# Kernel tuning notes

Measured on AMD Instinct MI355X. Metric: run time of the kernel, lower is better.

The kernel has to match this reference:

```python
import jax, jax.numpy as jnp
import numpy as np

K = 2
HD = 1024
IN = 784
NPARAMS = K + 2**K - 1  # 5
TRIL_R = np.array([0, 1, 1])  # tril_indices(2,2)
TRIL_C = np.array([0, 0, 1])


def setup_inputs() -> dict:
    key = jax.random.key(0)
    ks = jax.random.split(key, 8)
    B, T = 4096, 32
    s = 0.02
    return {
        "x": jax.random.normal(ks[0], (B, IN), jnp.float32),
        "hx": jnp.zeros((B, HD), jnp.float32),
        "eps": jax.random.normal(ks[1], (T, B, K), jnp.float32),
        "W_ih": jax.random.normal(ks[2], (HD, IN), jnp.float32) * s,
        "b_ih": jax.random.normal(ks[3], (HD,), jnp.float32) * s,
        "W_hh": jax.random.normal(ks[4], (HD, HD), jnp.float32) * s,
        "b_hh": jax.random.normal(ks[5], (HD,), jnp.float32) * s,
        "fe_W": jax.random.normal(ks[6], (NPARAMS, HD), jnp.float32) * s,
        "fe_b": jax.random.normal(ks[7], (NPARAMS,), jnp.float32) * s,
        "num_ticks": T,
    }


def _forward(x, hx, eps, W_ih, b_ih, W_hh, b_hh, fe_W, fe_b):
    B = x.shape[0]
    x_proj = x @ W_ih.T + b_ih  # invariant across ticks: [B, HD]
    diag = jnp.arange(K)

    def step(h, eps_t):
        h = jnp.tanh(x_proj + h @ W_hh.T + b_hh)  # RNNCell
        fe = h @ fe_W.T + fe_b                    # [B, NPARAMS]
        mus = fe[:, :K]
        sigmas = fe[:, K:]
        L = jnp.zeros((B, K, K), fe.dtype).at[:, TRIL_R, TRIL_C].set(sigmas)
        L = L.at[:, diag, diag].set(jax.nn.softplus(L[:, diag, diag]))
        z = mus + jnp.einsum('bij,bj->bi', L, eps_t)  # reparameterized sample
        return h, (z, L)

    _, (zs, Ls) = jax.lax.scan(step, hx, eps)  # zs: [T,B,K], Ls: [T,B,K,K]
    zs = jnp.transpose(zs, (1, 2, 0))          # [B, K, T]
    Ls = jnp.transpose(Ls, (1, 2, 3, 0))       # [B, K, K, T]
    # NOTE: original code stacks all_zs for both `zs` and `mus` (faithful to source).
    return zs, zs, Ls


def reference(x, hx, eps, W_ih, b_ih, W_hh, b_hh, fe_W, fe_b, num_ticks):
    eps = eps[:num_ticks]
    return _forward(x, hx, eps, W_ih, b_ih, W_hh, b_hh, fe_W, fe_b)
```

## Files before the change

kernel.cpp:

```cpp
#include <hip/hip_runtime.h>
#include <hip/hip_bf16.h>
#include <stdint.h>

#define B_ROWS 4096
#define HD 1024
#define IN_DIM 784
#define IN_PAD 832
#define T_TICKS 32

typedef float f32x4 __attribute__((ext_vector_type(4)));
typedef short short8 __attribute__((ext_vector_type(8)));
typedef __hip_bfloat16 bf16;

#define ABUF 8192

__device__ __forceinline__ float b2f(short s) {
  unsigned u = ((unsigned)(unsigned short)s) << 16;
  float f; __builtin_memcpy(&f, &u, 4); return f;
}

__device__ __forceinline__ float softplus_f(float x) {
  if (x > 20.f) return x;
  return log1pf(expf(x));
}

__device__ __forceinline__ float tanh_fast(float x) {
  x = fminf(fmaxf(x, -15.f), 15.f);
  float e = __expf(2.f * x);
  return (e - 1.f) / (e + 1.f);
}

__device__ __forceinline__ void gload_lds16(const void* g, void* l) {
  __builtin_amdgcn_global_load_lds(
      (const __attribute__((address_space(1))) uint32_t*)g,
      (__attribute__((address_space(3))) uint32_t*)l, 16, 0, 0);
}

__global__ __launch_bounds__(256) void conv_pad_kernel(
    const float* __restrict__ src, bf16* __restrict__ dst,
    int rows, int scols, int dcols) {
  int idx = blockIdx.x * 256 + threadIdx.x;
  int total = rows * dcols;
  if (idx >= total) return;
  int r = idx / dcols, c = idx - r * dcols;
  float v = (c < scols) ? src[(size_t)r * scols + c] : 0.f;
  dst[idx] = __float2bfloat16(v);
}

__global__ __launch_bounds__(256) void pack_w(
    const float* __restrict__ src, bf16* __restrict__ dst,
    int nkt, int scols) {
  int gid = blockIdx.x * 256 + threadIdx.x;
  int lane = gid & 63, f = gid >> 6;
  int total = 16 * nkt * 2 * 4;
  if (f >= total) return;
  int n = f & 3;
  int rest = f >> 2;
  int ks = rest & 1;
  int rest2 = rest >> 1;
  int kt = rest2 % nkt;
  int wnny = rest2 / nkt;
  int r = lane & 15, q = lane >> 4;
  int row = wnny * 64 + n * 16 + r;
  int k0 = kt * 64 + ks * 32 + q * 8;
  short8 v;
#pragma unroll
  for (int e = 0; e < 8; ++e) {
    int c = k0 + e;
    float x = (c < scols) ? src[(size_t)row * scols + c] : 0.f;
    bf16 b = __float2bfloat16(x);
    v[e] = *(short*)&b;
  }
  *(short8*)((char*)dst + (size_t)f * 1024 + lane * 16) = v;
}

__global__ __launch_bounds__(256) void pack_fe(
    const float* __restrict__ feW, bf16* __restrict__ dst) {
  int gid = blockIdx.x * 256 + threadIdx.x;
  int lane = gid & 63, f = gid >> 6;
  if (f >= 32) return;
  int ks = f & 1, kt = f >> 1;
  int r = lane & 15, q = lane >> 4;
  int k0 = kt * 64 + ks * 32 + q * 8;
  short8 v;
#pragma unroll
  for (int e = 0; e < 8; ++e) {
    float x = (r < 5) ? feW[(size_t)r * HD + k0 + e] : 0.f;
    bf16 b = __float2bfloat16(x);
    v[e] = *(short*)&b;
  }
  *(short8*)((char*)dst + (size_t)f * 1024 + lane * 16) = v;
}

template<int KDIM, int MODE>
__global__ __launch_bounds__(256) void gemm_core(
    const bf16* __restrict__ A,
    const bf16* __restrict__ Bpk,
    const bf16* __restrict__ feP,
    const float* __restrict__ bias1, const float* __restrict__ bias2,
    const bf16* __restrict__ xp, bf16* __restrict__ xp_out,
    bf16* __restrict__ outH, float* __restrict__ feRaw, int tprev)
{
  __shared__ char lds[2 * ABUF];
  const int tid = threadIdx.x;
  const int lane = tid & 63, w = tid >> 6;
  const int wm = w & 1, wn = w >> 1;
  const int l3 = lane >> 3, l7 = lane & 7;
  const int gcol = l7 ^ l3;
  const int r = lane & 15, q = lane >> 4;
  const int r7 = r & 7;
  const int lane16 = lane * 16;
  const int ldaB = KDIM * 2;
  const int NK = KDIM / 64;

  int bid = blockIdx.x;
  int v = (bid & 7) * 64 + (bid >> 3);
  const int mx = v >> 3, ny = v & 7;
  const int bm0 = mx * 64, bn0 = ny * 128;

  const bool feW0 = (MODE == 1) && (ny < 4) && (w == 0);

  f32x4 acc[2][4] = {};
  f32x4 acc_fe = {};

  const char* Asrc = (const char*)A + (size_t)(bm0 + l3) * ldaB + gcol * 16;
  const char* Bkt  = (const char*)Bpk + (size_t)(ny * 2 + wn) * NK * 8192;

  short8 Be[8], Bo[8], Bef[2], Bof[2];

#define STAGEA(buf, k)                                                         \
  {                                                                            \
    const char* Ak = Asrc + (size_t)(k) * 128;                                 \
    _Pragma("unroll") for (int j = 0; j < 2; ++j) {                            \
      int iA = w * 2 + j;                                                      \
      gload_lds16(Ak + (size_t)iA * 8 * ldaB, lds + (buf) * ABUF + iA * 1024); \
    }                                                                          \
  }

#define ISSUEB(BS, BSf, k)                                                     \
  {                                                                            \
    const char* bp = Bkt + (size_t)(k) * 8192;                                 \
    _Pragma("unroll") for (int i = 0; i < 8; ++i)                              \
      BS[i] = *(const short8*)(bp + i * 1024 + lane16);                        \
    if (feW0) {                                                                \
      const char* fp = (const char*)feP + (size_t)(k) * 2048;                  \
      BSf[0] = *(const short8*)(fp + lane16);                                  \
      BSf[1] = *(const short8*)(fp + 1024 + lane16);                           \
    }                                                                          \
  }

#define ITER(kp, BSc, BScf, BSn, BSnf)                                         \
  {                                                                            \
    const int _k = (kp);                                                       \
    if (_k + 1 < NK) {                                                         \
      STAGEA((_k + 1) & 1, _k + 1);                                            \
      ISSUEB(BSn, BSnf, _k + 1);                                               \
    }                                                                          \
    const char* lAb = lds + (_k & 1) * ABUF;                                   \
    short8 af[2][2], af_fe[2];                                                 \
    _Pragma("unroll") for (int ks = 0; ks < 2; ++ks) {                         \
      int sw = ((ks * 4 + q) ^ r7) << 4;                                       \
      _Pragma("unroll") for (int m = 0; m < 2; ++m)                            \
        af[ks][m] = *(const short8*)(lAb + (wm * 32 + m * 16 + r) * 128 + sw); \
    }                                                                          \
    if (feW0) {                                                                \
      _Pragma("unroll") for (int ks = 0; ks < 2; ++ks) {                       \
        int sw = ((ks * 4 + q) ^ r7) << 4;                                     \
        af_fe[ks] = *(const short8*)(lAb + (ny * 16 + r) * 128 + sw);          \
      }                                                                        \
    }                                                                          \
    _Pragma("unroll") for (int ks = 0; ks < 2; ++ks)                           \
      _Pragma("unroll") for (int m = 0; m < 2; ++m)                            \
        _Pragma("unroll") for (int n = 0; n < 4; ++n)                          \
          acc[m][n] = __builtin_amdgcn_mfma_f32_16x16x32_bf16(                 \
              af[ks][m], BSc[ks * 4 + n], acc[m][n], 0, 0, 0);                 \
    if (feW0) {                                                                \
      acc_fe = __builtin_amdgcn_mfma_f32_16x16x32_bf16(af_fe[0], BScf[0], acc_fe, 0, 0, 0); \
      acc_fe = __builtin_amdgcn_mfma_f32_16x16x32_bf16(af_fe[1], BScf[1], acc_fe, 0, 0, 0); \
    }                                                                          \
    __syncthreads();                                                           \
  }

  STAGEA(0, 0);
  ISSUEB(Be, Bef, 0);
  __syncthreads();

#pragma unroll
  for (int kt = 0; kt + 1 < NK; kt += 2) {
    ITER(kt,     Be, Bef, Bo, Bof);
    ITER(kt + 1, Bo, Bof, Be, Bef);
  }
  if (NK & 1) {
    ITER(NK - 1, Be, Bef, Bo, Bof);
  }
#undef ITER
#undef ISSUEB
#undef STAGEA

#pragma unroll
  for (int m = 0; m < 2; ++m) {
#pragma unroll
    for (int n = 0; n < 4; ++n) {
      int col = bn0 + wn * 64 + n * 16 + r;
#pragma unroll
      for (int i = 0; i < 4; ++i) {
        int row = bm0 + wm * 32 + m * 16 + q * 4 + i;
        float vv = acc[m][n][i];
        if (MODE == 0) {
          xp_out[(size_t)row * HD + col] = __float2bfloat16(vv + bias1[col] + bias2[col]);
        } else {
          float val = tanh_fast(vv + b2f(*(const short*)&xp[(size_t)row * HD + col]));
          outH[(size_t)row * HD + col] = __float2bfloat16(val);
        }
      }
    }
  }
  if (feW0 && tprev >= 0 && r < 5) {
#pragma unroll
    for (int i = 0; i < 4; ++i) {
      int rowg = bm0 + ny * 16 + q * 4 + i;
      feRaw[((size_t)rowg * T_TICKS + tprev) * 5 + r] = acc_fe[i];
    }
  }
}

__global__ __launch_bounds__(256) void fe_last(
    const bf16* __restrict__ h, const float* __restrict__ feW,
    float* __restrict__ feRaw)
{
  int wid = threadIdx.x >> 6, lane = threadIdx.x & 63;
  int b = blockIdx.x * 4 + wid;
  const bf16* hr = h + (size_t)b * HD + lane * 16;
  short8 hv0 = *(const short8*)hr;
  short8 hv1 = *(const short8*)(hr + 8);
  float hvf[16];
#pragma unroll
  for (int e = 0; e < 8; ++e) { hvf[e] = b2f(hv0[e]); hvf[8 + e] = b2f(hv1[e]); }

  float a0 = 0, a1 = 0, a2 = 0, a3 = 0, a4 = 0;
  int col0 = lane * 16;
#pragma unroll
  for (int e = 0; e < 16; ++e) {
    float hv = hvf[e];
    int col = col0 + e;
    a0 += hv * feW[0 * HD + col];
    a1 += hv * feW[1 * HD + col];
    a2 += hv * feW[2 * HD + col];
    a3 += hv * feW[3 * HD + col];
    a4 += hv * feW[4 * HD + col];
  }
#pragma unroll
  for (int off = 32; off >= 1; off >>= 1) {
    a0 += __shfl_xor(a0, off);
    a1 += __shfl_xor(a1, off);
    a2 += __shfl_xor(a2, off);
    a3 += __shfl_xor(a3, off);
    a4 += __shfl_xor(a4, off);
  }
  if (lane == 0) {
    float* fr = feRaw + ((size_t)b * T_TICKS + (T_TICKS - 1)) * 5;
    fr[0] = a0; fr[1] = a1; fr[2] = a2; fr[3] = a3; fr[4] = a4;
  }
}

__global__ __launch_bounds__(256) void finish_kernel(
    const float* __restrict__ feRaw, const float* __restrict__ feB,
    const float* __restrict__ eps, float* __restrict__ out)
{
  int gid = blockIdx.x * 256 + threadIdx.x;
  if (gid >= B_ROWS * T_TICKS) return;
  int b = gid >> 5, t = gid & 31;
  const float* fr = feRaw + ((size_t)b * T_TICKS + t) * 5;
  float mu0 = fr[0] + feB[0], mu1 = fr[1] + feB[1];
  float L00 = softplus_f(fr[2] + feB[2]);
  float L10 = fr[3] + feB[3];
  float L11 = softplus_f(fr[4] + feB[4]);
  const float* ep = eps + ((size_t)t * B_ROWS + b) * 2;
  float e0 = ep[0], e1 = ep[1];
  float z0 = mu0 + L00 * e0;
  float z1 = mu1 + L10 * e0 + L11 * e1;

  float* zs0 = out;
  float* zs1 = out + (size_t)B_ROWS * 2 * T_TICKS;
  float* Ls  = out + (size_t)2 * B_ROWS * 2 * T_TICKS;
  size_t zb = (size_t)b * 2 * T_TICKS + t;
  zs0[zb] = z0; zs0[zb + T_TICKS] = z1;
  zs1[zb] = z0; zs1[zb + T_TICKS] = z1;
  size_t lb = (size_t)b * 4 * T_TICKS + t;
  Ls[lb] = L00;
  Ls[lb + T_TICKS] = 0.f;
  Ls[lb + 2 * T_TICKS] = L10;
  Ls[lb + 3 * T_TICKS] = L11;
}

extern "C" void kernel_launch(void* const* d_in, const int* in_sizes, int n_in,
                              void* d_out, int out_size, void* d_ws, size_t ws_size,
                              hipStream_t stream) {
  const float* x    = (const float*)d_in[0];
  const float* hx   = (const float*)d_in[1];
  const float* eps  = (const float*)d_in[2];
  const float* W_ih = (const float*)d_in[3];
  const float* b_ih = (const float*)d_in[4];
  const float* W_hh = (const float*)d_in[5];
  const float* b_hh = (const float*)d_in[6];
  const float* fe_W = (const float*)d_in[7];
  const float* fe_b = (const float*)d_in[8];
  float* out = (float*)d_out;

  const int NKT_HH = HD / 64;
  const int NKT_IH = IN_PAD / 64;
  const int FR_HH = 16 * NKT_HH * 2 * 4;
  const int FR_IH = 16 * NKT_IH * 2 * 4;

  char* ws = (char*)d_ws;
  bf16* x_bf    = (bf16*)ws;  ws += (size_t)B_ROWS * IN_PAD * 2;
  bf16* hA      = (bf16*)ws;  ws += (size_t)B_ROWS * HD * 2;
  bf16* hB      = (bf16*)ws;  ws += (size_t)B_ROWS * HD * 2;
  bf16* xp_bf   = (bf16*)ws;  ws += (size_t)B_ROWS * HD * 2;
  bf16* pk_hh   = (bf16*)ws;  ws += (size_t)FR_HH * 1024;
  bf16* pk_ih   = (bf16*)ws;  ws += (size_t)FR_IH * 1024;
  bf16* feP     = (bf16*)ws;  ws += (size_t)32 * 1024;
  float* feRaw  = (float*)ws; ws += (size_t)B_ROWS * T_TICKS * 5 * 4;

  conv_pad_kernel<<<(B_ROWS * IN_PAD + 255) / 256, 256, 0, stream>>>(x, x_bf, B_ROWS, IN_DIM, IN_PAD);
  conv_pad_kernel<<<(B_ROWS * HD + 255) / 256, 256, 0, stream>>>(hx, hA, B_ROWS, HD, HD);
  pack_w<<<(FR_HH * 64 + 255) / 256, 256, 0, stream>>>(W_hh, pk_hh, NKT_HH, HD);
  pack_w<<<(FR_IH * 64 + 255) / 256, 256, 0, stream>>>(W_ih, pk_ih, NKT_IH, IN_DIM);
  pack_fe<<<(32 * 64 + 255) / 256, 256, 0, stream>>>(fe_W, feP);

  gemm_core<IN_PAD, 0><<<512, 256, 0, stream>>>(
      x_bf, pk_ih, nullptr, b_ih, b_hh,
      nullptr, xp_bf, nullptr, nullptr, -1);

  for (int t = 0; t < T_TICKS; ++t) {
    const bf16* hin = (t & 1) ? hB : hA;
    bf16* hout      = (t & 1) ? hA : hB;
    gemm_core<HD, 1><<<512, 256, 0, stream>>>(
        hin, pk_hh, feP, nullptr, nullptr,
        xp_bf, nullptr, hout, feRaw, t - 1);
  }
  fe_last<<<B_ROWS / 4, 256, 0, stream>>>(hA, fe_W, feRaw);
  finish_kernel<<<(B_ROWS * T_TICKS + 255) / 256, 256, 0, stream>>>(feRaw, fe_b, eps, out);
}
```

Baseline: 590.8 us.

## Use 128x128 tiles with intra-block split-K for the recurrent tick GEMM

Splits the per-tick recurrent GEMM into its own kernel. Each block now covers a 128x128 output tile with 512 threads instead of 64x128 with 256, and the grid shrinks from 512 to 256 blocks. The two halves of the waves each take half of every 64-wide K step, and their partial sums are reduced through LDS before the tanh epilogue. The aim is more reuse of A and B per block and less global traffic per output. The costs are a larger LDS footprint, an extra reduction pass, and fewer blocks in flight.

```diff
diff --git a/kernel.cpp b/kernel.cpp
--- a/kernel.cpp
+++ b/kernel.cpp
@@ -13,6 +13,8 @@
 typedef __hip_bfloat16 bf16;
 
 #define ABUF 8192
+#define TABUF 16384
+#define TLDS 66560
 
 __device__ __forceinline__ float b2f(short s) {
   unsigned u = ((unsigned)(unsigned short)s) << 16;
@@ -92,14 +94,12 @@
   *(short8*)((char*)dst + (size_t)f * 1024 + lane * 16) = v;
 }
 
-template<int KDIM, int MODE>
-__global__ __launch_bounds__(256) void gemm_core(
+template<int KDIM>
+__global__ __launch_bounds__(256) void gemm_xproj(
     const bf16* __restrict__ A,
     const bf16* __restrict__ Bpk,
-    const bf16* __restrict__ feP,
     const float* __restrict__ bias1, const float* __restrict__ bias2,
-    const bf16* __restrict__ xp, bf16* __restrict__ xp_out,
-    bf16* __restrict__ outH, float* __restrict__ feRaw, int tprev)
+    bf16* __restrict__ xp_out)
 {
   __shared__ char lds[2 * ABUF];
   const int tid = threadIdx.x;
@@ -118,108 +118,180 @@
   const int mx = v >> 3, ny = v & 7;
   const int bm0 = mx * 64, bn0 = ny * 128;
 
-  const bool feW0 = (MODE == 1) && (ny < 4) && (w == 0);
-
   f32x4 acc[2][4] = {};
-  f32x4 acc_fe = {};
-
   const char* Asrc = (const char*)A + (size_t)(bm0 + l3) * ldaB + gcol * 16;
   const char* Bkt  = (const char*)Bpk + (size_t)(ny * 2 + wn) * NK * 8192;
 
-  short8 Be[8], Bo[8], Bef[2], Bof[2];
-
-#define STAGEA(buf, k)                                                         \
-  {                                                                            \
-    const char* Ak = Asrc + (size_t)(k) * 128;                                 \
+  short8 Be[8], Bo[8];
+
+#define XSTAGE(buf, k)                                                         \
+  { const char* Ak = Asrc + (size_t)(k) * 128;                                 \
     _Pragma("unroll") for (int j = 0; j < 2; ++j) {                            \
       int iA = w * 2 + j;                                                      \
-      gload_lds16(Ak + (size_t)iA * 8 * ldaB, lds + (buf) * ABUF + iA * 1024); \
-    }                                                                          \
-  }
-
-#define ISSUEB(BS, BSf, k)                                                     \
-  {                                                                            \
-    const char* bp = Bkt + (size_t)(k) * 8192;                                 \
+      gload_lds16(Ak + (size_t)iA * 8 * ldaB, lds + (buf) * ABUF + iA * 1024); } }
+
+#define XISSUE(BS, k)                                                          \
+  { const char* bp = Bkt + (size_t)(k) * 8192;                                 \
     _Pragma("unroll") for (int i = 0; i < 8; ++i)                              \
-      BS[i] = *(const short8*)(bp + i * 1024 + lane16);                        \
-    if (feW0) {                                                                \
-      const char* fp = (const char*)feP + (size_t)(k) * 2048;                  \
-      BSf[0] = *(const short8*)(fp + lane16);                                  \
-      BSf[1] = *(const short8*)(fp + 1024 + lane16);                           \
-    }                                                                          \
-  }
-
-#define ITER(kp, BSc, BScf, BSn, BSnf)                                         \
-  {                                                                            \
-    const int _k = (kp);                                                       \
-    if (_k + 1 < NK) {                                                         \
-      STAGEA((_k + 1) & 1, _k + 1);                                            \
-      ISSUEB(BSn, BSnf, _k + 1);                                               \
-    }                                                                          \
+      BS[i] = *(const short8*)(bp + i * 1024 + lane16); }
+
+#define XITER(kp, BSc, BSn)                                                    \
+  { const int _k = (kp);                                                       \
+    if (_k + 1 < NK) { XSTAGE((_k + 1) & 1, _k + 1); XISSUE(BSn, _k + 1); }    \
     const char* lAb = lds + (_k & 1) * ABUF;                                   \
-    short8 af[2][2], af_fe[2];                                                 \
+    short8 af[2][2];                                                           \
     _Pragma("unroll") for (int ks = 0; ks < 2; ++ks) {                         \
       int sw = ((ks * 4 + q) ^ r7) << 4;                                       \
       _Pragma("unroll") for (int m = 0; m < 2; ++m)                            \
         af[ks][m] = *(const short8*)(lAb + (wm * 32 + m * 16 + r) * 128 + sw); \
-    }                                                                          \
-    if (feW0) {                                                                \
-      _Pragma("unroll") for (int ks = 0; ks < 2; ++ks) {                       \
-        int sw = ((ks * 4 + q) ^ r7) << 4;                                     \
-        af_fe[ks] = *(const short8*)(lAb + (ny * 16 + r) * 128 + sw);          \
-      }                                                                        \
     }                                                                          \
     _Pragma("unroll") for (int ks = 0; ks < 2; ++ks)                           \
       _Pragma("unroll") for (int m = 0; m < 2; ++m)                            \
         _Pragma("unroll") for (int n = 0; n < 4; ++n)                          \
           acc[m][n] = __builtin_amdgcn_mfma_f32_16x16x32_bf16(                 \
               af[ks][m], BSc[ks * 4 + n], acc[m][n], 0, 0, 0);                 \
-    if (feW0) {                                                                \
-      acc_fe = __builtin_amdgcn_mfma_f32_16x16x32_bf16(af_fe[0], BScf[0], acc_fe, 0, 0, 0); \
-      acc_fe = __builtin_amdgcn_mfma_f32_16x16x32_bf16(af_fe[1], BScf[1], acc_fe, 0, 0, 0); \
-    }                                                                          \
-    __syncthreads();                                                           \
-  }
-
-  STAGEA(0, 0);
-  ISSUEB(Be, Bef, 0);
+    __syncthreads(); }
+
+  XSTAGE(0, 0);
+  XISSUE(Be, 0);
   __syncthreads();
-
 #pragma unroll
   for (int kt = 0; kt + 1 < NK; kt += 2) {
-    ITER(kt,     Be, Bef, Bo, Bof);
-    ITER(kt + 1, Bo, Bof, Be, Bef);
-  }
-  if (NK & 1) {
-    ITER(NK - 1, Be, Bef, Bo, Bof);
-  }
-#undef ITER
-#undef ISSUEB
-#undef STAGEA
-
-#pragma unroll
-  for (int m = 0; m < 2; ++m) {
+    XITER(kt,     Be, Bo);
+    XITER(kt + 1, Bo, Be);
+  }
+  if (NK & 1) { XITER(NK - 1, Be, Bo); }
+#undef XITER
+#undef XISSUE
+#undef XSTAGE
+
+#pragma unroll
+  for (int m = 0; m < 2; ++m)
 #pragma unroll
     for (int n = 0; n < 4; ++n) {
       int col = bn0 + wn * 64 + n * 16 + r;
 #pragma unroll
       for (int i = 0; i < 4; ++i) {
         int row = bm0 + wm * 32 + m * 16 + q * 4 + i;
-        float vv = acc[m][n][i];
-        if (MODE == 0) {
-          xp_out[(size_t)row * HD + col] = __float2bfloat16(vv + bias1[col] + bias2[col]);
-        } else {
-          float val = tanh_fast(vv + b2f(*(const short*)&xp[(size_t)row * HD + col]));
-          outH[(size_t)row * HD + col] = __float2bfloat16(val);
+        xp_out[(size_t)row * HD + col] =
+            __float2bfloat16(acc[m][n][i] + bias1[col] + bias2[col]);
+      }
+    }
+}
+
+__global__ __launch_bounds__(512) void gemm_tick(
+    const bf16* __restrict__ hin,
+    const bf16* __restrict__ Bpk,
+    const bf16* __restrict__ feP,
+    const bf16* __restrict__ xp,
+    bf16* __restrict__ hout,
+    float* __restrict__ feRaw, int tprev)
+{
+  __shared__ char lds[TLDS];
+  const int tid = threadIdx.x;
+  const int lane = tid & 63, w = tid >> 6;
+  const int wm = w & 1, wn = (w >> 1) & 1, kh = w >> 2;
+  const int l3 = lane >> 3, l7 = lane & 7;
+  const int gcol = l7 ^ l3;
+  const int r = lane & 15, q = lane >> 4;
+  const int r7 = r & 7;
+  const int lane16 = lane * 16;
+  const int NKT = HD / 64;
+
+  int bid = blockIdx.x;
+  int v = (bid & 7) * 32 + (bid >> 3);
+  const int mx = v >> 3, ny = v & 7;
+  const int bm0 = mx * 128, bn0 = ny * 128;
+
+  const bool feB = ((w & 3) == 0);
+
+  f32x4 acc[4][4] = {};
+  f32x4 acc_fe = {};
+
+  const char* Asrc = (const char*)hin + (size_t)(bm0 + l3) * (HD * 2) + gcol * 16;
+  const char* Bkt  = (const char*)Bpk + (size_t)(ny * 2 + wn) * NKT * 8192;
+  const char* feC  = (const char*)feP;
+
+  short8 Be[4], Bo[4], Bef, Bof;
+
+#define TSTAGE(buf, k)                                                         \
+  { const char* Ak = Asrc + (size_t)(k) * 128;                                 \
+    _Pragma("unroll") for (int j = 0; j < 2; ++j) {                            \
+      int iA = w * 2 + j;                                                      \
+      gload_lds16(Ak + (size_t)iA * 8 * (HD * 2), lds + (buf) * TABUF + iA * 1024); } }
+
+#define TISSUE(BS, BSf, k)                                                     \
+  { const char* bp = Bkt + (size_t)(k) * 8192 + kh * 4096;                     \
+    _Pragma("unroll") for (int n = 0; n < 4; ++n)                              \
+      BS[n] = *(const short8*)(bp + n * 1024 + lane16);                        \
+    if (feB) BSf = *(const short8*)(feC + (size_t)(k) * 2048 + kh * 1024 + lane16); }
+
+#define TITER(kp, BSc, BScf, BSn, BSnf)                                        \
+  { const int _k = (kp);                                                       \
+    if (_k + 1 < NKT) { TSTAGE((_k + 1) & 1, _k + 1); TISSUE(BSn, BSnf, _k + 1); } \
+    const char* lAb = lds + (_k & 1) * TABUF;                                  \
+    const int sw = ((kh * 4 + q) ^ r7) << 4;                                   \
+    short8 af[4], af_fe;                                                       \
+    _Pragma("unroll") for (int m = 0; m < 4; ++m)                              \
+      af[m] = *(const short8*)(lAb + (wm * 64 + m * 16 + r) * 128 + sw);       \
+    if (feB) af_fe = *(const short8*)(lAb + (ny * 16 + r) * 128 + sw);         \
+    _Pragma("unroll") for (int m = 0; m < 4; ++m)                              \
+      _Pragma("unroll") for (int n = 0; n < 4; ++n)                            \
+        acc[m][n] = __builtin_amdgcn_mfma_f32_16x16x32_bf16(                   \
+            af[m], BSc[n], acc[m][n], 0, 0, 0);                                \
+    if (feB) acc_fe = __builtin_amdgcn_mfma_f32_16x16x32_bf16(af_fe, BScf, acc_fe, 0, 0, 0); \
+    __syncthreads(); }
+
+  TSTAGE(0, 0);
+  TISSUE(Be, Bef, 0);
+  __syncthreads();
+
+#pragma unroll
+  for (int kt = 0; kt + 1 < NKT; kt += 2) {
+    TITER(kt,     Be, Bef, Bo, Bof);
+    TITER(kt + 1, Bo, Bof, Be, Bef);
+  }
+#undef TITER
+#undef TISSUE
+#undef TSTAGE
+
+  if (kh == 1) {
+    char* reg = lds + (w - 4) * 16384;
+#pragma unroll
+    for (int m = 0; m < 4; ++m)
+#pragma unroll
+      for (int n = 0; n < 4; ++n)
+        *(f32x4*)(reg + (m * 4 + n) * 1024 + lane16) = acc[m][n];
+    if (feB) *(f32x4*)(lds + 65536 + lane16) = acc_fe;
+  }
+  __syncthreads();
+  if (kh == 0) {
+    char* reg = lds + w * 16384;
+#pragma unroll
+    for (int m = 0; m < 4; ++m)
+#pragma unroll
+      for (int n = 0; n < 4; ++n)
+        acc[m][n] += *(const f32x4*)(reg + (m * 4 + n) * 1024 + lane16);
+    if (feB) acc_fe += *(const f32x4*)(lds + 65536 + lane16);
+
+#pragma unroll
+    for (int m = 0; m < 4; ++m)
+#pragma unroll
+      for (int n = 0; n < 4; ++n) {
+        int col = bn0 + wn * 64 + n * 16 + r;
+#pragma unroll
+        for (int i = 0; i < 4; ++i) {
+          int row = bm0 + wm * 64 + m * 16 + q * 4 + i;
+          float val = tanh_fast(acc[m][n][i] + b2f(*(const short*)&xp[(size_t)row * HD + col]));
+          hout[(size_t)row * HD + col] = __float2bfloat16(val);
         }
       }
-    }
-  }
-  if (feW0 && tprev >= 0 && r < 5) {
-#pragma unroll
-    for (int i = 0; i < 4; ++i) {
-      int rowg = bm0 + ny * 16 + q * 4 + i;
-      feRaw[((size_t)rowg * T_TICKS + tprev) * 5 + r] = acc_fe[i];
+    if (feB && tprev >= 0 && r < 5) {
+#pragma unroll
+      for (int i = 0; i < 4; ++i) {
+        int rowg = bm0 + ny * 16 + q * 4 + i;
+        feRaw[((size_t)rowg * T_TICKS + tprev) * 5 + r] = acc_fe[i];
+      }
     }
   }
 }
@@ -328,16 +400,12 @@
   pack_w<<<(FR_IH * 64 + 255) / 256, 256, 0, stream>>>(W_ih, pk_ih, NKT_IH, IN_DIM);
   pack_fe<<<(32 * 64 + 255) / 256, 256, 0, stream>>>(fe_W, feP);
 
-  gemm_core<IN_PAD, 0><<<512, 256, 0, stream>>>(
-      x_bf, pk_ih, nullptr, b_ih, b_hh,
-      nullptr, xp_bf, nullptr, nullptr, -1);
+  gemm_xproj<IN_PAD><<<512, 256, 0, stream>>>(x_bf, pk_ih, b_ih, b_hh, xp_bf);
 
   for (int t = 0; t < T_TICKS; ++t) {
     const bf16* hin = (t & 1) ? hB : hA;
     bf16* hout      = (t & 1) ? hA : hB;
-    gemm_core<HD, 1><<<512, 256, 0, stream>>>(
-        hin, pk_hh, feP, nullptr, nullptr,
-        xp_bf, nullptr, hout, feRaw, t - 1);
+    gemm_tick<<<256, 512, 0, stream>>>(hin, pk_hh, feP, xp_bf, hout, feRaw, t - 1);
   }
   fe_last<<<B_ROWS / 4, 256, 0, stream>>>(hA, fe_W, feRaw);
   finish_kernel<<<(B_ROWS * T_TICKS + 255) / 256, 256, 0, stream>>>(feRaw, fe_b, eps, out);
```

Measured after the change: 633.9 us. +7.3%, slower.
